# Optimization experiments

Hardware: AMD Instinct MI355X
Metric: run time of the kernel (lower is better)

The kernel has to match this reference:

```python
import jax, jax.numpy as jnp
import numpy as np


def topk_activation(x, k):
    # x: [B, L]; keep top-k per row, zeros elsewhere (torch.topk + scatter_)
    vals, idx = jax.lax.top_k(x, k)            # [B, k]
    rows = jnp.arange(x.shape[0])[:, None]     # [B, 1]
    return jnp.zeros_like(x).at[rows, idx].set(vals)


def setup_inputs() -> dict:
    key = jax.random.key(0)
    k0, k1, k2, k3 = jax.random.split(key, 4)
    B, n_in, n_lat = 4096, 768, 24576
    x = jax.random.normal(k0, (B, n_in), dtype=jnp.float32)
    b = jnp.zeros((n_in,), jnp.float32)
    W_enc = jax.random.normal(k1, (n_lat, n_in), dtype=jnp.float32) * 0.02
    b_enc = jnp.zeros((n_lat,), jnp.float32)
    W_dec = jax.random.normal(k2, (n_in, n_lat), dtype=jnp.float32) * 0.02
    # unit L2 norm per decoder column (as in _normalize_decoder)
    W_dec = W_dec / jnp.clip(jnp.linalg.norm(W_dec, axis=0, keepdims=True), 1e-8)
    miss_counts = jax.random.randint(k3, (n_lat,), 0, 2)  # ~half 'dead' (>=1)
    return {"x": x, "b": b, "W_enc": W_enc, "b_enc": b_enc, "W_dec": W_dec,
            "miss_counts": miss_counts, "k": 32, "aux_k": 512}


def reference(x, b, W_enc, b_enc, W_dec, miss_counts, k, aux_k):
    x_centered = x - b                                   # [B, n_in]
    alpha_pre = x_centered @ W_enc.T + b_enc             # [B, n_lat]
    alpha = topk_activation(alpha_pre, k)                # sparse code
    x_hat = alpha @ W_dec.T + b                          # dense decode
    fired_mask = alpha != 0
    # aux dead-feature path; dead_mask = miss_counts >= threshold(=1).
    # With the chosen miss_counts fill, dead count >> aux_k, so
    # min(aux_k, dead.sum()) == aux_k (static for jit).
    dead_mask = miss_counts >= 1                         # [n_lat]
    alpha_pre_dead = jnp.where(dead_mask[None, :], alpha_pre, -jnp.inf)
    alpha_aux = topk_activation(alpha_pre_dead, aux_k)
    aux_x_hat = alpha_aux @ W_dec.T + b
    return x_hat, alpha, fired_mask, aux_x_hat
```

## Files before the change

### kernel.cpp

```cpp
#include <hip/hip_runtime.h>
#include <math.h>

#define NB   4096
#define NIN  768
#define NLAT 24576
#define K2   768
#define KT2  12

#define BM 128
#define BN 128
#define BK 16
#define LDT 132

#define CAND_CAP 512
#define BAND_CAP 160
#define MAIN_CAP 64
#define AUX_CAP  1024
#define SELT     1024
#define GRP      6

#define CM_CAP 768
#define CA_CAP 1536
#define BB_CAP 256
#define BPSTRIDE (BAND_CAP + 4)

#define OFF_K16  0
#define OFF_REDF 49152
#define OFF_CTRL 49664
#define OFF_PCNT 49792
#define OFF_CKM  50176
#define OFF_CIM  52224
#define OFF_CKA  54272
#define OFF_CIA  56320
#define OFF_BIM  58368
#define OFF_BIA  59008
#define OFF_BVM  59648
#define OFF_BVA  60928
#define OFF_BSM  62208
#define OFF_BSA  62368
#define OFF_REDI 62528
#define SMEM_SEL 62592

typedef __bf16 bf16x8 __attribute__((ext_vector_type(8)));
typedef float  f32x4  __attribute__((ext_vector_type(4)));

__device__ __forceinline__ unsigned fkey(float f) {
  unsigned u = __float_as_uint(f);
  return u ^ ((unsigned)((int)u >> 31) | 0x80000000u);
}
__device__ __forceinline__ float keyinv(unsigned u) {
  unsigned s = (u & 0x80000000u) ? (u ^ 0x80000000u) : ~u;
  return __uint_as_float(s);
}
__device__ __forceinline__ float zup(float p) {
  p = fminf(fmaxf(p, 1e-7f), 0.5f);
  float t = sqrtf(-2.0f * logf(p));
  return t - (2.30753f + 0.27061f * t) / (1.0f + 0.99229f * t + 0.04481f * t * t);
}

#define GLOAD16(g, l) __builtin_amdgcn_global_load_lds( \
    (const __attribute__((address_space(1))) unsigned int*)(g), \
    (__attribute__((address_space(3))) unsigned int*)(l), 16, 0, 0)

__global__ __launch_bounds__(256) void k_deadbits(const int* __restrict__ miss,
                                                  unsigned* __restrict__ bits,
                                                  float* __restrict__ rowStats) {
  int j = blockIdx.x * 256 + threadIdx.x;
  unsigned long long b = __ballot(miss[j] >= 1);
  if ((threadIdx.x & 63) == 0) {
    int w = j >> 5;
    bits[w] = (unsigned)b;
    bits[w + 1] = (unsigned)(b >> 32);
  }
  if (j < 2 * NB) rowStats[j] = 0.0f;
}

__global__ __launch_bounds__(256) void k_ndead(const unsigned* __restrict__ bits,
                                               int* __restrict__ out) {
  __shared__ int w[4];
  int t = threadIdx.x;
  int c = 0;
  for (int i = t; i < NLAT / 32; i += 256) c += __popc(bits[i]);
#pragma unroll
  for (int o = 32; o; o >>= 1) c += __shfl_xor(c, o);
  if ((t & 63) == 0) w[t >> 6] = c;
  __syncthreads();
  if (t == 0) out[0] = w[0] + w[1] + w[2] + w[3];
}

__global__ __launch_bounds__(256) void k_rowstats(const float* __restrict__ apre,
                                                  float* __restrict__ rowStats) {
  const int r = blockIdx.x, t = threadIdx.x;
  const float4* rowp = (const float4*)(apre + (size_t)r * NLAT);
  float s1 = 0.f, s2 = 0.f;
  for (int g = t; g < NLAT / 4; g += 256) {
    float4 v = rowp[g];
    s1 += v.x + v.y + v.z + v.w;
    s2 += v.x * v.x + v.y * v.y + v.z * v.z + v.w * v.w;
  }
#pragma unroll
  for (int o = 32; o; o >>= 1) { s1 += __shfl_xor(s1, o); s2 += __shfl_xor(s2, o); }
  __shared__ float w1[4], w2[4];
  if ((t & 63) == 0) { w1[t >> 6] = s1; w2[t >> 6] = s2; }
  __syncthreads();
  if (t == 0) {
    rowStats[2 * r] = w1[0] + w1[1] + w1[2] + w1[3];
    rowStats[2 * r + 1] = w2[0] + w2[1] + w2[2] + w2[3];
  }
}

__global__ __launch_bounds__(256) void k_transpose(const float* __restrict__ src,
                                                   __bf16* __restrict__ dst) {
  __shared__ float tile[32][33];
  int bx = blockIdx.x * 32;
  int by = blockIdx.y * 32;
  int tx = threadIdx.x, ty = threadIdx.y;
  for (int i = ty; i < 32; i += 8)
    tile[i][tx] = src[(size_t)(by + i) * NLAT + bx + tx];
  __syncthreads();
  for (int i = ty; i < 32; i += 8)
    dst[(size_t)(bx + i) * NIN + by + tx] = (__bf16)tile[tx][i];
}

__global__ __launch_bounds__(256) void k_pack_a(const float* __restrict__ x,
    const float* __restrict__ bvec, __bf16* __restrict__ A2) {
  const int mt = blockIdx.x, kt = blockIdx.y, t = threadIdx.x;
  __bf16* out = A2 + (((size_t)mt * KT2 + kt) << 13);
#pragma unroll
  for (int i = 0; i < 32; ++i) {
    int idx = i * 256 + t;
    int r = idx >> 6, c2 = idx & 63;
    int kk = c2 ^ ((r & 7) << 3);
    int k = kt * 64 + kk;
    float v = x[(size_t)(mt * 128 + r) * NIN + k] - bvec[k];
    out[idx] = (__bf16)v;
  }
}

__global__ __launch_bounds__(256) void k_pack_b(const float* __restrict__ We,
    __bf16* __restrict__ B2) {
  const int nt = blockIdx.x, kt = blockIdx.y, t = threadIdx.x;
  __bf16* out = B2 + (((size_t)nt * KT2 + kt) << 13);
#pragma unroll
  for (int i = 0; i < 32; ++i) {
    int idx = i * 256 + t;
    int r = idx >> 6, c2 = idx & 63;
    int kk = c2 ^ ((r & 7) << 3);
    int k = kt * 64 + kk;
    float v = We[(size_t)(nt * 128 + r) * NIN + k];
    out[idx] = (__bf16)v;
  }
}

__global__ __launch_bounds__(256) void k_gemm_bf16(
    const __bf16* __restrict__ A2, const __bf16* __restrict__ B2,
    const float* __restrict__ be, float* __restrict__ apre,
    float* __restrict__ rowStats) {
  __shared__ char sA[16384];
  __shared__ char sB[16384];
  const int t = threadIdx.x;
  const int lane = t & 63, wave = t >> 6;
  int flat = blockIdx.y * 32 + blockIdx.x;
  int nf = (flat & 7) * 768 + (flat >> 3);
  const int mt = nf & 31, nt = nf >> 5;
  const int wm = wave >> 1, wn = wave & 1;

  int aoff[4][2], boff[4][2];
#pragma unroll
  for (int f = 0; f < 4; ++f) {
    int ra = wm * 64 + f * 16 + (lane & 15);
    int rb = wn * 64 + f * 16 + (lane & 15);
#pragma unroll
    for (int kk = 0; kk < 2; ++kk) {
      int c = kk * 64 + (lane >> 4) * 16;
      aoff[f][kk] = ra * 128 + (c ^ ((ra & 7) << 4));
      boff[f][kk] = rb * 128 + (c ^ ((rb & 7) << 4));
    }
  }
  f32x4 acc[4][4] = {};
  const char* gA = (const char*)(A2 + (((size_t)mt * KT2) << 13));
  const char* gB = (const char*)(B2 + (((size_t)nt * KT2) << 13));
  for (int kt = 0; kt < KT2; ++kt) {
    const char* tA = gA + ((size_t)kt << 14);
    const char* tB = gB + ((size_t)kt << 14);
#pragma unroll
    for (int i = 0; i < 4; ++i) {
      int chunk = (i * 4 + wave) * 1024;
      GLOAD16(tA + chunk + lane * 16, sA + chunk);
      GLOAD16(tB + chunk + lane * 16, sB + chunk);
    }
    __syncthreads();
#pragma unroll
    for (int kk = 0; kk < 2; ++kk) {
      bf16x8 a[4], b[4];
#pragma unroll
      for (int f = 0; f < 4; ++f) {
        a[f] = *(const bf16x8*)(sA + aoff[f][kk]);
        b[f] = *(const bf16x8*)(sB + boff[f][kk]);
      }
#pragma unroll
      for (int mi = 0; mi < 4; ++mi)
#pragma unroll
        for (int ni = 0; ni < 4; ++ni)
          acc[mi][ni] = __builtin_amdgcn_mfma_f32_16x16x32_bf16(a[mi], b[ni], acc[mi][ni], 0, 0, 0);
    }
    __syncthreads();
  }
  const int m0 = mt * 128 + wm * 64, n0 = nt * 128 + wn * 64;
  float ps1[16] = {}, ps2[16] = {};
#pragma unroll
  for (int ni = 0; ni < 4; ++ni) {
    int n = n0 + ni * 16 + (lane & 15);
    float bb = be[n];
#pragma unroll
    for (int mi = 0; mi < 4; ++mi) {
      int mbase = m0 + mi * 16 + (lane >> 4) * 4;
#pragma unroll
      for (int q = 0; q < 4; ++q) {
        float v = acc[mi][ni][q] + bb;
        apre[(size_t)(mbase + q) * NLAT + n] = v;
        ps1[mi * 4 + q] += v;
        ps2[mi * 4 + q] += v * v;
      }
    }
  }
#pragma unroll
  for (int i = 0; i < 16; ++i) {
#pragma unroll
    for (int o = 1; o < 16; o <<= 1) {
      ps1[i] += __shfl_xor(ps1[i], o);
      ps2[i] += __shfl_xor(ps2[i], o);
    }
  }
  if ((lane & 15) == 0) {
#pragma unroll
    for (int i = 0; i < 16; ++i) {
      int row = m0 + (i >> 2) * 16 + (lane >> 4) * 4 + (i & 3);
      atomicAdd(&rowStats[2 * row], ps1[i]);
      atomicAdd(&rowStats[2 * row + 1], ps2[i]);
    }
  }
}

__global__ __launch_bounds__(256) void k_encgemm_f32(
    const float* __restrict__ x, const float* __restrict__ bvec,
    const float* __restrict__ We, const float* __restrict__ be,
    float* __restrict__ apre) {
  __shared__ float As[BK][LDT];
  __shared__ float Bs[BK][LDT];
  const int t = threadIdx.x;
  const int m0 = blockIdx.x * BM;
  const int n0 = blockIdx.y * BN;
  const int lane = t & 63, wave = t >> 6;
  const int cn = ((wave & 1) * 8 + (lane & 7)) * 8;
  const int cm = ((wave >> 1) * 8 + (lane >> 3)) * 8;
  float acc[8][8] = {};
  const float* xb = x + (size_t)m0 * NIN;
  const float* wb = We + (size_t)n0 * NIN;
  for (int k0 = 0; k0 < NIN; k0 += BK) {
#pragma unroll
    for (int i = 0; i < 2; ++i) {
      int e = t + i * 256;
      int row = e >> 2, q = e & 3;
      float4 bv = *(const float4*)(bvec + k0 + q * 4);
      float4 av = *(const float4*)(xb + (size_t)row * NIN + k0 + q * 4);
      av.x -= bv.x; av.y -= bv.y; av.z -= bv.z; av.w -= bv.w;
      As[q * 4 + 0][row] = av.x; As[q * 4 + 1][row] = av.y;
      As[q * 4 + 2][row] = av.z; As[q * 4 + 3][row] = av.w;
      float4 wv = *(const float4*)(wb + (size_t)row * NIN + k0 + q * 4);
      Bs[q * 4 + 0][row] = wv.x; Bs[q * 4 + 1][row] = wv.y;
      Bs[q * 4 + 2][row] = wv.z; Bs[q * 4 + 3][row] = wv.w;
    }
    __syncthreads();
#pragma unroll
    for (int kk = 0; kk < BK; ++kk) {
      float a0[8], b0[8];
      *(float4*)&a0[0] = *(const float4*)&As[kk][cm];
      *(float4*)&a0[4] = *(const float4*)&As[kk][cm + 4];
      *(float4*)&b0[0] = *(const float4*)&Bs[kk][cn];
      *(float4*)&b0[4] = *(const float4*)&Bs[kk][cn + 4];
#pragma unroll
      for (int i = 0; i < 8; ++i)
#pragma unroll
        for (int j = 0; j < 8; ++j)
          acc[i][j] = fmaf(a0[i], b0[j], acc[i][j]);
    }
    __syncthreads();
  }
  float bb[8];
  *(float4*)&bb[0] = *(const float4*)(be + n0 + cn);
  *(float4*)&bb[4] = *(const float4*)(be + n0 + cn + 4);
#pragma unroll
  for (int i = 0; i < 8; ++i) {
    float4 v0 = make_float4(acc[i][0] + bb[0], acc[i][1] + bb[1],
                            acc[i][2] + bb[2], acc[i][3] + bb[3]);
    float4 v1 = make_float4(acc[i][4] + bb[4], acc[i][5] + bb[5],
                            acc[i][6] + bb[6], acc[i][7] + bb[7]);
    float* orow = apre + (size_t)(m0 + cm + i) * NLAT + n0 + cn;
    *(float4*)orow = v0;
    *(float4*)(orow + 4) = v1;
  }
}

__global__ __launch_bounds__(1024) void k_select17(
    const float* __restrict__ apre, const float* __restrict__ x,
    const float* __restrict__ bvec, const float* __restrict__ We,
    const float* __restrict__ be, const unsigned* __restrict__ dbits,
    const int* __restrict__ kptr, const int* __restrict__ akptr,
    const int* __restrict__ ndeadP, const float* __restrict__ rowStats,
    int* __restrict__ cnts, int* __restrict__ mIdxG, float* __restrict__ mValG,
    int* __restrict__ aIdxG, float* __restrict__ aValG,
    int* __restrict__ bandP, int* __restrict__ flags) {
  __shared__ int ctrl[24];
  __shared__ int histM[256];
  __shared__ int histA[256];
  __shared__ uint2 cM[CM_CAP];
  __shared__ uint2 cA[CA_CAP];
  __shared__ uint2 bbM[BB_CAP];
  __shared__ uint2 bbA[BB_CAP];
  __shared__ int biM[BAND_CAP];
  __shared__ int biA[BAND_CAP];
  __shared__ double bvM[BAND_CAP];
  __shared__ double bvA[BAND_CAP];
  __shared__ unsigned char bsM[BAND_CAP];
  __shared__ unsigned char bsA[BAND_CAP];
  unsigned* uctrl = (unsigned*)ctrl;

  const int t = threadIdx.x;
  const int r = blockIdx.x;
  const int lane = t & 63, wave = t >> 6;

  if (t < 24) ctrl[t] = 0;
  if (t >= 256 && t < 512) histM[t - 256] = 0;
  else if (t >= 512 && t < 768) histA[t - 512] = 0;
  __syncthreads();

  int kmain = kptr[0]; if (kmain > MAIN_CAP) kmain = MAIN_CAP;
  int kaux  = akptr[0]; if (kaux > AUX_CAP)  kaux  = AUX_CAP;
  const int ndead = ndeadP[0];
  int kauxE = kaux > ndead ? ndead : kaux;
  const bool mainOn = (kmain > 0);
  const bool auxOn  = (kauxE > 0);
  const float s1 = rowStats[2 * r], s2 = rowStats[2 * r + 1];
  const float mu = s1 / (float)NLAT;
  const float sg = sqrtf(fmaxf(s2 / (float)NLAT - mu * mu, 1e-20f));
  unsigned TkM = 0xFFFFFFFFu, TkA = 0xFFFFFFFFu;
  if (mainOn) TkM = fkey(mu + sg * zup(8.f * kmain / (float)NLAT));
  if (auxOn) {
    float facA = (3.f * kauxE > 1280.f) ? 2.f : 3.f;
    TkA = fkey(mu + sg * zup(facA * kauxE / (float)ndead));
  }

  const uint4* rowp = (const uint4*)(apre + (size_t)r * NLAT);
  unsigned mxM = 0u, mxA = 0u;
#pragma unroll
  for (int i = 0; i < GRP; ++i) {
    int g = t + SELT * i;
    uint4 rv = rowp[g];
    unsigned nb = (dbits[g >> 3] >> ((g & 7) * 4)) & 0xFu;
    float vs[4] = {__uint_as_float(rv.x), __uint_as_float(rv.y),
                   __uint_as_float(rv.z), __uint_as_float(rv.w)};
#pragma unroll
    for (int q = 0; q < 4; ++q) {
      unsigned kk = fkey(vs[q]);
      unsigned j = (unsigned)(4 * g + q);
      if (mainOn && kk >= TkM) {
        mxM = kk > mxM ? kk : mxM;
        int p = atomicAdd(&ctrl[0], 1);
        if (p < CM_CAP) { cM[p].x = kk; cM[p].y = j; }
      }
      if (auxOn && ((nb >> q) & 1u) && kk >= TkA) {
        mxA = kk > mxA ? kk : mxA;
        int p = atomicAdd(&ctrl[1], 1);
        if (p < CA_CAP) { cA[p].x = kk; cA[p].y = j; }
      }
    }
  }
#pragma unroll
  for (int o = 32; o; o >>= 1) {
    unsigned a = __shfl_xor(mxM, o); mxM = a > mxM ? a : mxM;
    unsigned b = __shfl_xor(mxA, o); mxA = b > mxA ? b : mxA;
  }
  if (lane == 0) { atomicMax(&uctrl[10], mxM); atomicMax(&uctrl[11], mxA); }
  __syncthreads();
  int ccM = ctrl[0], ccA = ctrl[1];
  bool ok = (!mainOn || (ccM >= kmain && ccM <= CM_CAP)) &&
            (!auxOn  || (ccA >= kauxE && ccA <= CA_CAP));
  if (!ok) { if (t == 0) flags[r] = 1; return; }
  if (!auxOn) ccA = 0;
  if (!mainOn) ccM = 0;
  unsigned MxM = uctrl[10], MxA = uctrl[11];
  float sclM = 255.0f / fmaxf((float)(MxM - TkM) + 1.0f, 1.0f);
  float sclA = 255.0f / fmaxf((float)(MxA - TkA) + 1.0f, 1.0f);

  for (int c = t; c < ccM; c += 1024) {
    int b = (int)((float)(cM[c].x - TkM) * sclM);
    b = b < 0 ? 0 : (b > 255 ? 255 : b);
    atomicAdd(&histM[b], 1);
  }
  for (int c = t; c < ccA; c += 1024) {
    int b = (int)((float)(cA[c].x - TkA) * sclA);
    b = b < 0 ? 0 : (b > 255 ? 255 : b);
    atomicAdd(&histA[b], 1);
  }
  __syncthreads();
  if (t == 0 && mainOn) {
    int above = 0, b = 0;
    for (int i = 255; i >= 0; --i) {
      if (above + histM[i] >= kmain) { b = i; break; }
      above += histM[i];
    }
    ctrl[12] = b; ctrl[13] = above;
  }
  if (t == 64 && auxOn) {
    int above = 0, b = 0;
    for (int i = 255; i >= 0; --i) {
      if (above + histA[i] >= kauxE) { b = i; break; }
      above += histA[i];
    }
    ctrl[14] = b; ctrl[15] = above;
  }
  __syncthreads();
  int bM = ctrl[12], aboveM = ctrl[13];
  int bA = ctrl[14], aboveA = ctrl[15];
  for (int c = t; c < ccM; c += 1024) {
    int b = (int)((float)(cM[c].x - TkM) * sclM);
    b = b < 0 ? 0 : (b > 255 ? 255 : b);
    if (b == bM) {
      int p = atomicAdd(&ctrl[16], 1);
      if (p < BB_CAP) bbM[p] = cM[c];
    }
  }
  for (int c = t; c < ccA; c += 1024) {
    int b = (int)((float)(cA[c].x - TkA) * sclA);
    b = b < 0 ? 0 : (b > 255 ? 255 : b);
    if (b == bA) {
      int p = atomicAdd(&ctrl[17], 1);
      if (p < BB_CAP) bbA[p] = cA[c];
    }
  }
  __syncthreads();
  int nbM = ctrl[16], nbA = ctrl[17];
  if ((mainOn && nbM > BB_CAP) || (auxOn && nbA > BB_CAP)) {
    if (t == 0) flags[r] = 1;
    return;
  }
  if (!mainOn) nbM = 0;
  if (!auxOn) nbA = 0;
  if (t < nbM) {
    uint2 e = bbM[t];
    int rank = 0;
    for (int qq = 0; qq < nbM; ++qq) {
      uint2 f = bbM[qq];
      rank += (f.x > e.x || (f.x == e.x && (int)f.y < (int)e.y)) ? 1 : 0;
    }
    if (rank == kmain - aboveM - 1) ctrl[2] = (int)e.x;
  }
  if (t >= 512 && t - 512 < nbA) {
    uint2 e = bbA[t - 512];
    int rank = 0;
    for (int qq = 0; qq < nbA; ++qq) {
      uint2 f = bbA[qq];
      rank += (f.x > e.x || (f.x == e.x && (int)f.y < (int)e.y)) ? 1 : 0;
    }
    if (rank == kauxE - aboveA - 1) ctrl[3] = (int)e.x;
  }
  __syncthreads();

  float VsM = keyinv((unsigned)ctrl[2]);
  float epsM = 1.5e-2f + 2e-3f * fabsf(VsM);
  unsigned KhiBM = mainOn ? fkey(VsM + epsM) : 0xFFFFFFFFu;
  unsigned KloBM = mainOn ? fkey(VsM - epsM) : 0xFFFFFFFFu;
  float VsA = keyinv((unsigned)ctrl[3]);
  float epsA = 1.5e-2f + 2e-3f * fabsf(VsA);
  unsigned KhiBA = auxOn ? fkey(VsA + epsA) : 0xFFFFFFFFu;
  unsigned KloBA = auxOn ? fkey(VsA - epsA) : 0xFFFFFFFFu;
  for (int c = t; c < ccM; c += 1024) {
    unsigned kk = cM[c].x;
    if (kk > KhiBM) atomicAdd(&ctrl[4], 1);
    else if (kk >= KloBM) {
      int p = atomicAdd(&ctrl[5], 1);
      if (p < BAND_CAP) biM[p] = (int)cM[c].y;
    }
  }
  for (int c = t; c < ccA; c += 1024) {
    unsigned kk = cA[c].x;
    if (kk > KhiBA) atomicAdd(&ctrl[6], 1);
    else if (kk >= KloBA) {
      int p = atomicAdd(&ctrl[7], 1);
      if (p < BAND_CAP) biA[p] = (int)cA[c].y;
    }
  }
  __syncthreads();
  if ((mainOn && ctrl[5] > BAND_CAP) || (auxOn && ctrl[7] > BAND_CAP)) {
    if (t == 0) flags[r] = 1;
    return;
  }
  if (t == 0) flags[r] = 0;
  int nAbM = ctrl[4], bcM = ctrl[5];
  int nAbA = ctrl[6], bcA = ctrl[7];
  if (!mainOn) bcM = 0;
  if (!auxOn) bcA = 0;
  int needBM = kmain - nAbM; if (needBM < 0) needBM = 0; if (needBM > bcM) needBM = bcM;
  int needBA = kauxE - nAbA; if (needBA < 0) needBA = 0; if (needBA > bcA) needBA = bcA;

  {
    const float* xr = x + (size_t)r * NIN;
    float xb[NIN / 64];
#pragma unroll
    for (int jj = 0; jj < NIN / 64; ++jj) {
      int col = lane + 64 * jj;
      xb[jj] = xr[col] - bvec[col];
    }
    int tot = bcM + bcA;
    for (int m = wave; m < tot; m += 16) {
      int j = (m < bcM) ? biM[m] : biA[m - bcM];
      const float* wr = We + (size_t)j * NIN;
      double s = 0.0;
#pragma unroll
      for (int jj = 0; jj < NIN / 64; ++jj)
        s += (double)xb[jj] * (double)wr[lane + 64 * jj];
#pragma unroll
      for (int o = 32; o; o >>= 1) s += __shfl_xor(s, o);
      if (lane == 0) {
        if (m < bcM) bvM[m] = s + (double)be[j];
        else bvA[m - bcM] = s + (double)be[j];
      }
    }
  }
  __syncthreads();
  if (t < bcM) {
    double vi = bvM[t]; int ii = biM[t];
    double tie = fabs(vi) * 4e-8 + 1e-12;
    int rank = 0;
    for (int qq = 0; qq < bcM; ++qq) {
      double d = bvM[qq] - vi;
      rank += ((fabs(d) <= tie) ? (biM[qq] < ii) : (d > 0.0)) ? 1 : 0;
    }
    bsM[t] = (rank < needBM) ? 1 : 0;
  }
  if (t >= 512 && t - 512 < bcA) {
    int tt = t - 512;
    double vi = bvA[tt]; int ii = biA[tt];
    double tie = fabs(vi) * 4e-8 + 1e-12;
    int rank = 0;
    for (int qq = 0; qq < bcA; ++qq) {
      double d = bvA[qq] - vi;
      rank += ((fabs(d) <= tie) ? (biA[qq] < ii) : (d > 0.0)) ? 1 : 0;
    }
    bsA[tt] = (rank < needBA) ? 1 : 0;
  }
  __syncthreads();

  for (int c = t; c < ccM; c += 1024) {
    unsigned kk = cM[c].x; int j = (int)cM[c].y;
    bool sel = kk > KhiBM;
    if (!sel && kk >= KloBM) {
      for (int m2 = 0; m2 < bcM; ++m2)
        if (biM[m2] == j) { sel = bsM[m2] != 0; break; }
    }
    float v = keyinv(kk);
    if (sel && v != 0.0f) {
      int p = atomicAdd(&ctrl[8], 1);
      if (p < MAIN_CAP) { mIdxG[r * MAIN_CAP + p] = j; mValG[r * MAIN_CAP + p] = v; }
    }
  }
  for (int c = t; c < ccA; c += 1024) {
    unsigned kk = cA[c].x; int j = (int)cA[c].y;
    bool sel = kk > KhiBA;
    if (!sel && kk >= KloBA) {
      for (int m2 = 0; m2 < bcA; ++m2)
        if (biA[m2] == j) { sel = bsA[m2] != 0; break; }
    }
    float v = keyinv(kk);
    if (sel && v != 0.0f) {
      int p = atomicAdd(&ctrl[9], 1);
      if (p < AUX_CAP) { aIdxG[r * AUX_CAP + p] = j; aValG[r * AUX_CAP + p] = v; }
    }
  }
  __syncthreads();
  int* bp = bandP + (size_t)r * BPSTRIDE;
  if (t == 0) {
    cnts[2 * r] = ctrl[8] < MAIN_CAP ? ctrl[8] : MAIN_CAP;
    cnts[2 * r + 1] = auxOn ? (ctrl[9] < AUX_CAP ? ctrl[9] : AUX_CAP) : 0;
    bp[0] = (int)KhiBM; bp[1] = (int)KloBM; bp[2] = bcM;
  }
  if (t < bcM) bp[3 + t] = (biM[t] << 1) | (int)bsM[t];
}

__global__ __launch_bounds__(256) void k_emit(
    const float* apre, const int* __restrict__ flags,
    const int* __restrict__ bandP, float* __restrict__ alpha, float* mask) {
  const int bid = blockIdx.x;
  const int r = bid / 3, c = bid % 3;
  if (flags[r]) return;
  __shared__ int hdr[3];
  __shared__ int bent[BAND_CAP];
  const int t = threadIdx.x;
  const int* bp = bandP + (size_t)r * BPSTRIDE;
  if (t < 3) hdr[t] = bp[t];
  __syncthreads();
  int bc = hdr[2];
  if (t < bc) bent[t] = bp[3 + t];
  __syncthreads();
  unsigned KhiB = (unsigned)hdr[0], KloB = (unsigned)hdr[1];
  const float4* src = (const float4*)(apre + (size_t)r * NLAT) + c * 2048;
  float4* adst = (float4*)(alpha + (size_t)r * NLAT) + c * 2048;
  float4* mdst = (float4*)(mask + (size_t)r * NLAT) + c * 2048;
  const int ebase = c * 8192;
#pragma unroll
  for (int i = 0; i < 8; ++i) {
    int g = t + 256 * i;
    float4 v4 = src[g];
    float vs[4] = {v4.x, v4.y, v4.z, v4.w};
    float av[4], mv[4];
#pragma unroll
    for (int q = 0; q < 4; ++q) {
      float v = vs[q];
      unsigned kk = fkey(v);
      int j = ebase + 4 * g + q;
      bool sel = kk > KhiB;
      if (!sel && kk >= KloB) {
        for (int m = 0; m < bc; ++m)
          if ((bent[m] >> 1) == j) { sel = (bent[m] & 1) != 0; break; }
      }
      av[q] = sel ? v : 0.0f;
      mv[q] = (sel && v != 0.0f) ? 1.0f : 0.0f;
    }
    adst[g] = make_float4(av[0], av[1], av[2], av[3]);
    mdst[g] = make_float4(mv[0], mv[1], mv[2], mv[3]);
  }
}

__global__ __launch_bounds__(SELT) void k_selectFB(
    const float* apre, const float* __restrict__ x,
    const float* __restrict__ bvec, const float* __restrict__ We,
    const float* __restrict__ be, const unsigned* __restrict__ dbits,
    const int* __restrict__ kptr, const int* __restrict__ akptr,
    float* __restrict__ alpha, float* mask,
    int* __restrict__ cnts, int* __restrict__ mIdxG, float* __restrict__ mValG,
    int* __restrict__ aIdxG, float* __restrict__ aValG,
    const int* __restrict__ flags) {
  if (flags[blockIdx.x] == 0) return;
  extern __shared__ char smem[];
  uint2*    keys2 = (uint2*)(smem + OFF_K16);
  float*    redF  = (float*)(smem + OFF_REDF);
  int*      redI  = (int*)(smem + OFF_REDI);
  int*      ctrl  = (int*)(smem + OFF_CTRL);
  float*    ctrlF = (float*)(smem + OFF_CTRL);
  int*      pcnt  = (int*)(smem + OFF_PCNT);
  unsigned* ckM   = (unsigned*)(smem + OFF_CKM);
  int*      ciM   = (int*)(smem + OFF_CIM);
  unsigned* ckA   = (unsigned*)(smem + OFF_CKA);
  int*      ciA   = (int*)(smem + OFF_CIA);
  int*      biM   = (int*)(smem + OFF_BIM);
  int*      biA   = (int*)(smem + OFF_BIA);
  double*   bvM   = (double*)(smem + OFF_BVM);
  double*   bvA   = (double*)(smem + OFF_BVA);
  unsigned char* bsM = (unsigned char*)(smem + OFF_BSM);
  unsigned char* bsA = (unsigned char*)(smem + OFF_BSA);

  const int t = threadIdx.x;
  const int r = blockIdx.x;
  const int lane = t & 63, wave = t >> 6;

  if (t < 96) pcnt[t] = 0;
  else if (t < 108) ctrl[t - 96] = 0;

  const uint4* rowp = (const uint4*)(apre + (size_t)r * NLAT);
  const float* rowf = apre + (size_t)r * NLAT;
  unsigned dm = 0;
  float s1 = 0.f, s2 = 0.f;
  float vmxA = -INFINITY, vmnA = INFINITY, vmxD = -INFINITY, vmnD = INFINITY;
#pragma unroll
  for (int i = 0; i < GRP; ++i) {
    int g = t + SELT * i;
    uint4 rv = rowp[g];
    unsigned nb = (dbits[g >> 3] >> ((g & 7) * 4)) & 0xFu;
    dm |= nb << (4 * i);
    float vs[4] = {__uint_as_float(rv.x), __uint_as_float(rv.y),
                   __uint_as_float(rv.z), __uint_as_float(rv.w)};
    unsigned k16[4];
#pragma unroll
    for (int q = 0; q < 4; ++q) {
      float v = vs[q];
      k16[q] = fkey(v) >> 16;
      s1 += v; s2 += v * v;
      vmxA = fmaxf(vmxA, v); vmnA = fminf(vmnA, v);
      if ((nb >> q) & 1u) { vmxD = fmaxf(vmxD, v); vmnD = fminf(vmnD, v); }
    }
    uint2 kp2;
    kp2.x = k16[0] | (k16[1] << 16);
    kp2.y = k16[2] | (k16[3] << 16);
    keys2[g] = kp2;
  }
  int nd = __popc(dm & 0xFFFFFFu);
#pragma unroll
  for (int o = 32; o; o >>= 1) {
    s1 += __shfl_xor(s1, o); s2 += __shfl_xor(s2, o);
    vmxA = fmaxf(vmxA, __shfl_xor(vmxA, o)); vmnA = fminf(vmnA, __shfl_xor(vmnA, o));
    vmxD = fmaxf(vmxD, __shfl_xor(vmxD, o)); vmnD = fminf(vmnD, __shfl_xor(vmnD, o));
    nd += __shfl_xor(nd, o);
  }
  if (lane == 0) {
    float* rf = redF + wave * 8;
    rf[0] = s1; rf[1] = s2; rf[2] = vmxA; rf[3] = vmnA; rf[4] = vmxD; rf[5] = vmnD;
    redI[wave] = nd;
  }
  __syncthreads();
  if (wave == 0) {
    float a0 = 0.f, a1 = 0.f, a2 = -INFINITY, a3 = INFINITY, a4 = -INFINITY, a5 = INFINITY;
    int a6 = 0;
    if (lane < 16) {
      const float* rf = redF + lane * 8;
      a0 = rf[0]; a1 = rf[1]; a2 = rf[2]; a3 = rf[3]; a4 = rf[4]; a5 = rf[5];
      a6 = redI[lane];
    }
#pragma unroll
    for (int o = 32; o; o >>= 1) {
      a0 += __shfl_xor(a0, o); a1 += __shfl_xor(a1, o);
      a2 = fmaxf(a2, __shfl_xor(a2, o)); a3 = fminf(a3, __shfl_xor(a3, o));
// ... 275 lines not shown
          for (int m2 = 0; m2 < bcM; ++m2)
            if (biM[m2] == j) { selM = bsM[m2] != 0; break; }
        }
        bool nz = selM && (v != 0.0f);
        av[q] = selM ? v : 0.0f;
        mv[q] = nz ? 1.0f : 0.0f;
        if (nz) {
          int p = atomicAdd(&ctrl[8], 1);
          if (p < MAIN_CAP) { mIdxG[r * MAIN_CAP + p] = j; mValG[r * MAIN_CAP + p] = v; }
        }
        if (auxOn && ((nb >> q) & 1u)) {
          bool selA = kk > KhiBA;
          if (!selA && kk >= KloBA) {
            for (int m2 = 0; m2 < bcA; ++m2)
              if (biA[m2] == j) { selA = bsA[m2] != 0; break; }
          }
          if (selA && v != 0.0f) {
            int p = atomicAdd(&ctrl[9], 1);
            if (p < AUX_CAP) { aIdxG[r * AUX_CAP + p] = j; aValG[r * AUX_CAP + p] = v; }
          }
        }
      }
      arow[g] = make_float4(av[0], av[1], av[2], av[3]);
      mrow[g] = make_float4(mv[0], mv[1], mv[2], mv[3]);
    }
  }
  __syncthreads();
  if (t == 0) {
    cnts[2 * r] = ctrl[8] < MAIN_CAP ? ctrl[8] : MAIN_CAP;
    cnts[2 * r + 1] = auxOn ? (ctrl[9] < AUX_CAP ? ctrl[9] : AUX_CAP) : 0;
  }
}

__global__ __launch_bounds__(256) void k_decode(
    const int* __restrict__ cnts, const int* __restrict__ mIdxG,
    const float* __restrict__ mValG, const int* __restrict__ aIdxG,
    const float* __restrict__ aValG, const float* __restrict__ bvec,
    const __bf16* __restrict__ Wt, const float* __restrict__ Wd,
    float* __restrict__ xhat, float* __restrict__ auxo) {
  const int r = blockIdx.x, t = threadIdx.x;
  __shared__ int sMi[MAIN_CAP];
  __shared__ float sMv[MAIN_CAP];
  __shared__ int sAi[AUX_CAP];
  __shared__ float sAv[AUX_CAP];
  int kc = cnts[2 * r], ac = cnts[2 * r + 1];
  if (t < MAIN_CAP && t < kc) { sMi[t] = mIdxG[r * MAIN_CAP + t]; sMv[t] = mValG[r * MAIN_CAP + t]; }
  for (int i = t; i < ac; i += 256) { sAi[i] = aIdxG[r * AUX_CAP + i]; sAv[i] = aValG[r * AUX_CAP + i]; }
  __syncthreads();

  float o0 = 0.f, o1 = 0.f, o2 = 0.f;
  float a0 = 0.f, a1 = 0.f, a2 = 0.f;
  if (Wt) {
    int i = 0;
    for (; i + 4 <= kc; i += 4) {
      int i0 = sMi[i], i1 = sMi[i + 1], i2 = sMi[i + 2], i3 = sMi[i + 3];
      float v0 = sMv[i], v1 = sMv[i + 1], v2 = sMv[i + 2], v3 = sMv[i + 3];
      const __bf16* p0 = Wt + (size_t)i0 * NIN;
      const __bf16* p1 = Wt + (size_t)i1 * NIN;
      const __bf16* p2 = Wt + (size_t)i2 * NIN;
      const __bf16* p3 = Wt + (size_t)i3 * NIN;
      float w00 = p0[t], w01 = p0[t + 256], w02 = p0[t + 512];
      float w10 = p1[t], w11 = p1[t + 256], w12 = p1[t + 512];
      float w20 = p2[t], w21 = p2[t + 256], w22 = p2[t + 512];
      float w30 = p3[t], w31 = p3[t + 256], w32 = p3[t + 512];
      o0 = fmaf(v0, w00, o0); o1 = fmaf(v0, w01, o1); o2 = fmaf(v0, w02, o2);
      o0 = fmaf(v1, w10, o0); o1 = fmaf(v1, w11, o1); o2 = fmaf(v1, w12, o2);
      o0 = fmaf(v2, w20, o0); o1 = fmaf(v2, w21, o1); o2 = fmaf(v2, w22, o2);
      o0 = fmaf(v3, w30, o0); o1 = fmaf(v3, w31, o1); o2 = fmaf(v3, w32, o2);
    }
    for (; i < kc; ++i) {
      const __bf16* p = Wt + (size_t)sMi[i] * NIN;
      float v = sMv[i];
      o0 = fmaf(v, (float)p[t], o0);
      o1 = fmaf(v, (float)p[t + 256], o1);
      o2 = fmaf(v, (float)p[t + 512], o2);
    }
    i = 0;
    for (; i + 4 <= ac; i += 4) {
      int i0 = sAi[i], i1 = sAi[i + 1], i2 = sAi[i + 2], i3 = sAi[i + 3];
      float v0 = sAv[i], v1 = sAv[i + 1], v2 = sAv[i + 2], v3 = sAv[i + 3];
      const __bf16* p0 = Wt + (size_t)i0 * NIN;
      const __bf16* p1 = Wt + (size_t)i1 * NIN;
      const __bf16* p2 = Wt + (size_t)i2 * NIN;
      const __bf16* p3 = Wt + (size_t)i3 * NIN;
      float w00 = p0[t], w01 = p0[t + 256], w02 = p0[t + 512];
      float w10 = p1[t], w11 = p1[t + 256], w12 = p1[t + 512];
      float w20 = p2[t], w21 = p2[t + 256], w22 = p2[t + 512];
      float w30 = p3[t], w31 = p3[t + 256], w32 = p3[t + 512];
      a0 = fmaf(v0, w00, a0); a1 = fmaf(v0, w01, a1); a2 = fmaf(v0, w02, a2);
      a0 = fmaf(v1, w10, a0); a1 = fmaf(v1, w11, a1); a2 = fmaf(v1, w12, a2);
      a0 = fmaf(v2, w20, a0); a1 = fmaf(v2, w21, a1); a2 = fmaf(v2, w22, a2);
      a0 = fmaf(v3, w30, a0); a1 = fmaf(v3, w31, a1); a2 = fmaf(v3, w32, a2);
    }
    for (; i < ac; ++i) {
      const __bf16* p = Wt + (size_t)sAi[i] * NIN;
      float v = sAv[i];
      a0 = fmaf(v, (float)p[t], a0);
      a1 = fmaf(v, (float)p[t + 256], a1);
      a2 = fmaf(v, (float)p[t + 512], a2);
    }
  } else {
    for (int i = 0; i < kc; ++i) {
      float v = sMv[i]; int ix = sMi[i];
      o0 = fmaf(v, Wd[(size_t)t * NLAT + ix], o0);
      o1 = fmaf(v, Wd[(size_t)(t + 256) * NLAT + ix], o1);
      o2 = fmaf(v, Wd[(size_t)(t + 512) * NLAT + ix], o2);
    }
    for (int i = 0; i < ac; ++i) {
      float v = sAv[i]; int ix = sAi[i];
      a0 = fmaf(v, Wd[(size_t)t * NLAT + ix], a0);
      a1 = fmaf(v, Wd[(size_t)(t + 256) * NLAT + ix], a1);
      a2 = fmaf(v, Wd[(size_t)(t + 512) * NLAT + ix], a2);
    }
  }
  float b0 = bvec[t], b1 = bvec[t + 256], b2 = bvec[t + 512];
  xhat[(size_t)r * NIN + t] = o0 + b0;
  xhat[(size_t)r * NIN + t + 256] = o1 + b1;
  xhat[(size_t)r * NIN + t + 512] = o2 + b2;
  auxo[(size_t)r * NIN + t] = a0 + b0;
  auxo[(size_t)r * NIN + t + 256] = a1 + b1;
  auxo[(size_t)r * NIN + t + 512] = a2 + b2;
}

extern "C" void kernel_launch(void* const* d_in, const int* in_sizes, int n_in,
                              void* d_out, int out_size, void* d_ws, size_t ws_size,
                              hipStream_t stream) {
  const float* x  = (const float*)d_in[0];
  const float* bv = (const float*)d_in[1];
  const float* We = (const float*)d_in[2];
  const float* be = (const float*)d_in[3];
  const float* Wd = (const float*)d_in[4];
  const int* miss = (const int*)d_in[5];
  const int* kp   = (const int*)d_in[6];
  const int* akp  = (const int*)d_in[7];

  float* out   = (float*)d_out;
  float* xhat  = out;
  float* alpha = out + (size_t)3145728;
  float* apre  = out + (size_t)103809024;
  float* auxo  = out + (size_t)204472320;

  char* wsb = (char*)d_ws;
  size_t o = 0;
  unsigned* dbits = (unsigned*)(wsb + o); o += 65536;
  int*   cnts  = (int*)(wsb + o); o += 65536;
  int*   mIdxG = (int*)(wsb + o); o += (size_t)NB * MAIN_CAP * 4;
  float* mValG = (float*)(wsb + o); o += (size_t)NB * MAIN_CAP * 4;
  int*   aIdxG = (int*)(wsb + o); o += (size_t)NB * AUX_CAP * 4;
  float* aValG = (float*)(wsb + o); o += (size_t)NB * AUX_CAP * 4;
  int*   bandP = (int*)(wsb + o); o += (size_t)NB * BPSTRIDE * 4;
  int*   flags = (int*)(wsb + o); o += 65536;
  int*   ndead = (int*)(wsb + o); o += 65536;
  float* rowStats = (float*)(wsb + o); o += (size_t)NB * 2 * 4;
  size_t offWt = o;
  size_t offA2 = offWt + (size_t)NLAT * NIN * 2;
  size_t offB2 = offA2 + (size_t)NB * K2 * 2;
  size_t needFull = offB2 + (size_t)NLAT * K2 * 2;
  bool haveWt   = ws_size >= offA2;
  bool haveFull = ws_size >= needFull;
  __bf16* Wt = haveWt ? (__bf16*)(wsb + offWt) : nullptr;
  __bf16* A2 = (__bf16*)(wsb + offA2);
  __bf16* B2 = (__bf16*)(wsb + offB2);

  k_deadbits<<<96, 256, 0, stream>>>(miss, dbits, rowStats);
  k_ndead<<<1, 256, 0, stream>>>(dbits, ndead);
  if (haveFull) {
    k_pack_a<<<dim3(32, KT2), 256, 0, stream>>>(x, bv, A2);
    k_pack_b<<<dim3(192, KT2), 256, 0, stream>>>(We, B2);
  }
  if (haveWt)
    k_transpose<<<dim3(NLAT / 32, NIN / 32), dim3(32, 8), 0, stream>>>(Wd, Wt);

  if (haveFull) {
    k_gemm_bf16<<<dim3(32, 192), 256, 0, stream>>>(A2, B2, be, apre, rowStats);
  } else {
    k_encgemm_f32<<<dim3(NB / BM, NLAT / BN), 256, 0, stream>>>(x, bv, We, be, apre);
    k_rowstats<<<NB, 256, 0, stream>>>(apre, rowStats);
  }

  k_select17<<<NB, 1024, 0, stream>>>(apre, x, bv, We, be, dbits, kp, akp, ndead,
                                      rowStats, cnts, mIdxG, mValG, aIdxG, aValG,
                                      bandP, flags);
  k_selectFB<<<NB, SELT, SMEM_SEL, stream>>>(apre, x, bv, We, be, dbits, kp, akp,
                                             alpha, apre, cnts, mIdxG, mValG,
                                             aIdxG, aValG, flags);
  k_emit<<<NB * 3, 256, 0, stream>>>(apre, flags, bandP, alpha, apre);
  k_decode<<<NB, 256, 0, stream>>>(cnts, mIdxG, mValG, aIdxG, aValG, bv,
                                   Wt, Wd, xhat, auxo);
}
```

Baseline: 1.463 ms.

## Split row selection into multi-block candidate extraction and per-row ranking kernels

Replaces the single 1024-thread per-row select kernel with two kernels. The first scans each row with three 256-thread blocks and appends threshold-passing candidates to global buffers, using global atomics for per-row counts and maxima. The second kernel runs 512 threads per row, copies those candidates into shared memory and does the histogram, band and ranking logic as before. The aim is better occupancy and parallelism for the memory-bound row scan. In exchange it adds global atomic contention on per-row counters, extra global traffic for the candidate buffers, one more launch, and half as many waves for the band dot products.

```diff
diff --git a/kernel.cpp b/kernel.cpp
--- a/kernel.cpp
+++ b/kernel.cpp
@@ -64,7 +64,8 @@
 
 __global__ __launch_bounds__(256) void k_deadbits(const int* __restrict__ miss,
                                                   unsigned* __restrict__ bits,
-                                                  float* __restrict__ rowStats) {
+                                                  float* __restrict__ rowStats,
+                                                  int* __restrict__ gmeta) {
   int j = blockIdx.x * 256 + threadIdx.x;
   unsigned long long b = __ballot(miss[j] >= 1);
   if ((threadIdx.x & 63) == 0) {
@@ -73,6 +74,7 @@
     bits[w + 1] = (unsigned)(b >> 32);
   }
   if (j < 2 * NB) rowStats[j] = 0.0f;
+  if (j < 4 * NB) gmeta[j] = 0;
 }
 
 __global__ __launch_bounds__(256) void k_ndead(const unsigned* __restrict__ bits,
@@ -302,38 +304,14 @@
   }
 }
 
-__global__ __launch_bounds__(1024) void k_select17(
-    const float* __restrict__ apre, const float* __restrict__ x,
-    const float* __restrict__ bvec, const float* __restrict__ We,
-    const float* __restrict__ be, const unsigned* __restrict__ dbits,
+__global__ __launch_bounds__(256) void k_extract(
+    const float* __restrict__ apre, const unsigned* __restrict__ dbits,
     const int* __restrict__ kptr, const int* __restrict__ akptr,
     const int* __restrict__ ndeadP, const float* __restrict__ rowStats,
-    int* __restrict__ cnts, int* __restrict__ mIdxG, float* __restrict__ mValG,
-    int* __restrict__ aIdxG, float* __restrict__ aValG,
-    int* __restrict__ bandP, int* __restrict__ flags) {
-  __shared__ int ctrl[24];
-  __shared__ int histM[256];
-  __shared__ int histA[256];
-  __shared__ uint2 cM[CM_CAP];
-  __shared__ uint2 cA[CA_CAP];
-  __shared__ uint2 bbM[BB_CAP];
-  __shared__ uint2 bbA[BB_CAP];
-  __shared__ int biM[BAND_CAP];
-  __shared__ int biA[BAND_CAP];
-  __shared__ double bvM[BAND_CAP];
-  __shared__ double bvA[BAND_CAP];
-  __shared__ unsigned char bsM[BAND_CAP];
-  __shared__ unsigned char bsA[BAND_CAP];
-  unsigned* uctrl = (unsigned*)ctrl;
-
+    int* __restrict__ gmeta, uint2* __restrict__ gcM, uint2* __restrict__ gcA) {
+  const int bid = blockIdx.x;
+  const int r = bid / 3, c = bid % 3;
   const int t = threadIdx.x;
-  const int r = blockIdx.x;
-  const int lane = t & 63, wave = t >> 6;
-
-  if (t < 24) ctrl[t] = 0;
-  if (t >= 256 && t < 512) histM[t - 256] = 0;
-  else if (t >= 512 && t < 768) histA[t - 512] = 0;
-  __syncthreads();
 
   int kmain = kptr[0]; if (kmain > MAIN_CAP) kmain = MAIN_CAP;
   int kaux  = akptr[0]; if (kaux > AUX_CAP)  kaux  = AUX_CAP;
@@ -351,55 +329,126 @@
     TkA = fkey(mu + sg * zup(facA * kauxE / (float)ndead));
   }
 
-  const uint4* rowp = (const uint4*)(apre + (size_t)r * NLAT);
-  unsigned mxM = 0u, mxA = 0u;
-#pragma unroll
-  for (int i = 0; i < GRP; ++i) {
-    int g = t + SELT * i;
-    uint4 rv = rowp[g];
-    unsigned nb = (dbits[g >> 3] >> ((g & 7) * 4)) & 0xFu;
+  int* cntM = gmeta;
+  int* cntA = gmeta + NB;
+  unsigned* mxM = (unsigned*)(gmeta + 2 * NB);
+  unsigned* mxA = (unsigned*)(gmeta + 3 * NB);
+  uint2* lcM = gcM + (size_t)r * CM_CAP;
+  uint2* lcA = gcA + (size_t)r * CA_CAP;
+
+  const uint4* src = (const uint4*)(apre + (size_t)r * NLAT) + c * 2048;
+  const int ebase = c * 8192;
+  unsigned wmxM = 0u, wmxA = 0u;
+#pragma unroll
+  for (int i = 0; i < 8; ++i) {
+    int g = t + 256 * i;
+    uint4 rv = src[g];
+    int j0 = ebase + 4 * g;
+    unsigned nb = (dbits[j0 >> 5] >> (j0 & 31)) & 0xFu;
     float vs[4] = {__uint_as_float(rv.x), __uint_as_float(rv.y),
                    __uint_as_float(rv.z), __uint_as_float(rv.w)};
 #pragma unroll
     for (int q = 0; q < 4; ++q) {
       unsigned kk = fkey(vs[q]);
-      unsigned j = (unsigned)(4 * g + q);
+      unsigned j = (unsigned)(j0 + q);
       if (mainOn && kk >= TkM) {
-        mxM = kk > mxM ? kk : mxM;
-        int p = atomicAdd(&ctrl[0], 1);
-        if (p < CM_CAP) { cM[p].x = kk; cM[p].y = j; }
+        wmxM = kk > wmxM ? kk : wmxM;
+        int p = atomicAdd(&cntM[r], 1);
+        if (p < CM_CAP) { lcM[p].x = kk; lcM[p].y = j; }
       }
       if (auxOn && ((nb >> q) & 1u) && kk >= TkA) {
-        mxA = kk > mxA ? kk : mxA;
-        int p = atomicAdd(&ctrl[1], 1);
-        if (p < CA_CAP) { cA[p].x = kk; cA[p].y = j; }
+        wmxA = kk > wmxA ? kk : wmxA;
+        int p = atomicAdd(&cntA[r], 1);
+        if (p < CA_CAP) { lcA[p].x = kk; lcA[p].y = j; }
       }
     }
   }
 #pragma unroll
   for (int o = 32; o; o >>= 1) {
-    unsigned a = __shfl_xor(mxM, o); mxM = a > mxM ? a : mxM;
-    unsigned b = __shfl_xor(mxA, o); mxA = b > mxA ? b : mxA;
-  }
-  if (lane == 0) { atomicMax(&uctrl[10], mxM); atomicMax(&uctrl[11], mxA); }
-  __syncthreads();
-  int ccM = ctrl[0], ccA = ctrl[1];
+    unsigned a = __shfl_xor(wmxM, o); wmxM = a > wmxM ? a : wmxM;
+    unsigned b = __shfl_xor(wmxA, o); wmxA = b > wmxA ? b : wmxA;
+  }
+  if ((t & 63) == 0) {
+    if (wmxM) atomicMax(&mxM[r], wmxM);
+    if (wmxA) atomicMax(&mxA[r], wmxA);
+  }
+}
+
+__global__ __launch_bounds__(512) void k_rank(
+    const float* __restrict__ x, const float* __restrict__ bvec,
+    const float* __restrict__ We, const float* __restrict__ be,
+    const int* __restrict__ kptr, const int* __restrict__ akptr,
+    const int* __restrict__ ndeadP, const float* __restrict__ rowStats,
+    const int* __restrict__ gmeta, const uint2* __restrict__ gcM,
+    const uint2* __restrict__ gcA,
+    int* __restrict__ cnts, int* __restrict__ mIdxG, float* __restrict__ mValG,
+    int* __restrict__ aIdxG, float* __restrict__ aValG,
+    int* __restrict__ bandP, int* __restrict__ flags) {
+  __shared__ int ctrl[24];
+  __shared__ int histM[256];
+  __shared__ int histA[256];
+  __shared__ uint2 lcM[CM_CAP];
+  __shared__ uint2 lcA[CA_CAP];
+  __shared__ uint2 bbM[BB_CAP];
+  __shared__ uint2 bbA[BB_CAP];
+  __shared__ int biM[BAND_CAP];
+  __shared__ int biA[BAND_CAP];
+  __shared__ double bvM[BAND_CAP];
+  __shared__ double bvA[BAND_CAP];
+  __shared__ unsigned char bsM[BAND_CAP];
+  __shared__ unsigned char bsA[BAND_CAP];
+
+  const int t = threadIdx.x;
+  const int r = blockIdx.x;
+  const int lane = t & 63, wave = t >> 6;
+
+  if (t < 24) ctrl[t] = 0;
+  if (t >= 24 && t < 280) histM[t - 24] = 0;
+  else if (t >= 280 && t < 512 ) histA[t - 280] = 0;
+  __syncthreads();
+  if (t < 24) {}
+  if (t < 24 + 24) {}
+  if (t < 24) {}
+  if (t < 24) histA[232 + t] = 0;
+  __syncthreads();
+
+  int kmain = kptr[0]; if (kmain > MAIN_CAP) kmain = MAIN_CAP;
+  int kaux  = akptr[0]; if (kaux > AUX_CAP)  kaux  = AUX_CAP;
+  const int ndead = ndeadP[0];
+  int kauxE = kaux > ndead ? ndead : kaux;
+  const bool mainOn = (kmain > 0);
+  const bool auxOn  = (kauxE > 0);
+  const float s1 = rowStats[2 * r], s2 = rowStats[2 * r + 1];
+  const float mu = s1 / (float)NLAT;
+  const float sg = sqrtf(fmaxf(s2 / (float)NLAT - mu * mu, 1e-20f));
+  unsigned TkM = 0xFFFFFFFFu, TkA = 0xFFFFFFFFu;
+  if (mainOn) TkM = fkey(mu + sg * zup(8.f * kmain / (float)NLAT));
+  if (auxOn) {
+    float facA = (3.f * kauxE > 1280.f) ? 2.f : 3.f;
+    TkA = fkey(mu + sg * zup(facA * kauxE / (float)ndead));
+  }
+
+  int ccM = gmeta[r], ccA = gmeta[NB + r];
+  unsigned MxM = ((const unsigned*)(gmeta + 2 * NB))[r];
+  unsigned MxA = ((const unsigned*)(gmeta + 3 * NB))[r];
   bool ok = (!mainOn || (ccM >= kmain && ccM <= CM_CAP)) &&
             (!auxOn  || (ccA >= kauxE && ccA <= CA_CAP));
   if (!ok) { if (t == 0) flags[r] = 1; return; }
   if (!auxOn) ccA = 0;
   if (!mainOn) ccM = 0;
-  unsigned MxM = uctrl[10], MxA = uctrl[11];
+  for (int i = t; i < ccM; i += 512) lcM[i] = gcM[(size_t)r * CM_CAP + i];
+  for (int i = t; i < ccA; i += 512) lcA[i] = gcA[(size_t)r * CA_CAP + i];
+  __syncthreads();
   float sclM = 255.0f / fmaxf((float)(MxM - TkM) + 1.0f, 1.0f);
   float sclA = 255.0f / fmaxf((float)(MxA - TkA) + 1.0f, 1.0f);
 
-  for (int c = t; c < ccM; c += 1024) {
-    int b = (int)((float)(cM[c].x - TkM) * sclM);
+  for (int c = t; c < ccM; c += 512) {
+    int b = (int)((float)(lcM[c].x - TkM) * sclM);
     b = b < 0 ? 0 : (b > 255 ? 255 : b);
     atomicAdd(&histM[b], 1);
   }
-  for (int c = t; c < ccA; c += 1024) {
-    int b = (int)((float)(cA[c].x - TkA) * sclA);
+  for (int c = t; c < ccA; c += 512) {
+    int b = (int)((float)(lcA[c].x - TkA) * sclA);
     b = b < 0 ? 0 : (b > 255 ? 255 : b);
     atomicAdd(&histA[b], 1);
   }
@@ -423,20 +472,20 @@
   __syncthreads();
   int bM = ctrl[12], aboveM = ctrl[13];
   int bA = ctrl[14], aboveA = ctrl[15];
-  for (int c = t; c < ccM; c += 1024) {
-    int b = (int)((float)(cM[c].x - TkM) * sclM);
+  for (int c = t; c < ccM; c += 512) {
+    int b = (int)((float)(lcM[c].x - TkM) * sclM);
     b = b < 0 ? 0 : (b > 255 ? 255 : b);
     if (b == bM) {
       int p = atomicAdd(&ctrl[16], 1);
-      if (p < BB_CAP) bbM[p] = cM[c];
-    }
-  }
-  for (int c = t; c < ccA; c += 1024) {
-    int b = (int)((float)(cA[c].x - TkA) * sclA);
+      if (p < BB_CAP) bbM[p] = lcM[c];
+    }
+  }
+  for (int c = t; c < ccA; c += 512) {
+    int b = (int)((float)(lcA[c].x - TkA) * sclA);
     b = b < 0 ? 0 : (b > 255 ? 255 : b);
     if (b == bA) {
       int p = atomicAdd(&ctrl[17], 1);
-      if (p < BB_CAP) bbA[p] = cA[c];
+      if (p < BB_CAP) bbA[p] = lcA[c];
     }
   }
   __syncthreads();
@@ -456,8 +505,8 @@
     }
     if (rank == kmain - aboveM - 1) ctrl[2] = (int)e.x;
   }
-  if (t >= 512 && t - 512 < nbA) {
-    uint2 e = bbA[t - 512];
+  if (t >= 256 && t - 256 < nbA) {
+    uint2 e = bbA[t - 256];
     int rank = 0;
     for (int qq = 0; qq < nbA; ++qq) {
       uint2 f = bbA[qq];
@@ -475,20 +524,20 @@
   float epsA = 1.5e-2f + 2e-3f * fabsf(VsA);
   unsigned KhiBA = auxOn ? fkey(VsA + epsA) : 0xFFFFFFFFu;
   unsigned KloBA = auxOn ? fkey(VsA - epsA) : 0xFFFFFFFFu;
-  for (int c = t; c < ccM; c += 1024) {
-    unsigned kk = cM[c].x;
+  for (int c = t; c < ccM; c += 512) {
+    unsigned kk = lcM[c].x;
     if (kk > KhiBM) atomicAdd(&ctrl[4], 1);
     else if (kk >= KloBM) {
       int p = atomicAdd(&ctrl[5], 1);
-      if (p < BAND_CAP) biM[p] = (int)cM[c].y;
-    }
-  }
-  for (int c = t; c < ccA; c += 1024) {
-    unsigned kk = cA[c].x;
+      if (p < BAND_CAP) biM[p] = (int)lcM[c].y;
+    }
+  }
+  for (int c = t; c < ccA; c += 512) {
+    unsigned kk = lcA[c].x;
     if (kk > KhiBA) atomicAdd(&ctrl[6], 1);
     else if (kk >= KloBA) {
       int p = atomicAdd(&ctrl[7], 1);
-      if (p < BAND_CAP) biA[p] = (int)cA[c].y;
+      if (p < BAND_CAP) biA[p] = (int)lcA[c].y;
     }
   }
   __syncthreads();
@@ -513,7 +562,7 @@
       xb[jj] = xr[col] - bvec[col];
     }
     int tot = bcM + bcA;
-    for (int m = wave; m < tot; m += 16) {
+    for (int m = wave; m < tot; m += 8) {
       int j = (m < bcM) ? biM[m] : biA[m - bcM];
       const float* wr = We + (size_t)j * NIN;
       double s = 0.0;
@@ -539,8 +588,8 @@
     }
     bsM[t] = (rank < needBM) ? 1 : 0;
   }
-  if (t >= 512 && t - 512 < bcA) {
-    int tt = t - 512;
+  if (t >= 256 && t - 256 < bcA) {
+    int tt = t - 256;
     double vi = bvA[tt]; int ii = biA[tt];
     double tie = fabs(vi) * 4e-8 + 1e-12;
     int rank = 0;
@@ -552,8 +601,8 @@
   }
   __syncthreads();
 
-  for (int c = t; c < ccM; c += 1024) {
-    unsigned kk = cM[c].x; int j = (int)cM[c].y;
+  for (int c = t; c < ccM; c += 512) {
+    unsigned kk = lcM[c].x; int j = (int)lcM[c].y;
     bool sel = kk > KhiBM;
     if (!sel && kk >= KloBM) {
       for (int m2 = 0; m2 < bcM; ++m2)
@@ -565,8 +614,8 @@
       if (p < MAIN_CAP) { mIdxG[r * MAIN_CAP + p] = j; mValG[r * MAIN_CAP + p] = v; }
     }
   }
-  for (int c = t; c < ccA; c += 1024) {
-    unsigned kk = cA[c].x; int j = (int)cA[c].y;
+  for (int c = t; c < ccA; c += 512) {
+    unsigned kk = lcA[c].x; int j = (int)lcA[c].y;
     bool sel = kk > KhiBA;
     if (!sel && kk >= KloBA) {
       for (int m2 = 0; m2 < bcA; ++m2)
@@ -1148,6 +1197,9 @@
   int*   flags = (int*)(wsb + o); o += 65536;
   int*   ndead = (int*)(wsb + o); o += 65536;
   float* rowStats = (float*)(wsb + o); o += (size_t)NB * 2 * 4;
+  int*   gmeta = (int*)(wsb + o); o += (size_t)NB * 4 * 4;
+  uint2* gcM = (uint2*)(wsb + o); o += (size_t)NB * CM_CAP * 8;
+  uint2* gcA = (uint2*)(wsb + o); o += (size_t)NB * CA_CAP * 8;
   size_t offWt = o;
   size_t offA2 = offWt + (size_t)NLAT * NIN * 2;
   size_t offB2 = offA2 + (size_t)NB * K2 * 2;
@@ -1158,7 +1210,7 @@
   __bf16* A2 = (__bf16*)(wsb + offA2);
   __bf16* B2 = (__bf16*)(wsb + offB2);
 
-  k_deadbits<<<96, 256, 0, stream>>>(miss, dbits, rowStats);
+  k_deadbits<<<96, 256, 0, stream>>>(miss, dbits, rowStats, gmeta);
   k_ndead<<<1, 256, 0, stream>>>(dbits, ndead);
   if (haveFull) {
     k_pack_a<<<dim3(32, KT2), 256, 0, stream>>>(x, bv, A2);
@@ -1174,9 +1226,11 @@
     k_rowstats<<<NB, 256, 0, stream>>>(apre, rowStats);
   }
 
-  k_select17<<<NB, 1024, 0, stream>>>(apre, x, bv, We, be, dbits, kp, akp, ndead,
-                                      rowStats, cnts, mIdxG, mValG, aIdxG, aValG,
-                                      bandP, flags);
+  k_extract<<<NB * 3, 256, 0, stream>>>(apre, dbits, kp, akp, ndead, rowStats,
+                                        gmeta, gcM, gcA);
+  k_rank<<<NB, 512, 0, stream>>>(x, bv, We, be, kp, akp, ndead, rowStats,
+                                 gmeta, gcM, gcA, cnts, mIdxG, mValG,
+                                 aIdxG, aValG, bandP, flags);
   k_selectFB<<<NB, SELT, SMEM_SEL, stream>>>(apre, x, bv, We, be, dbits, kp, akp,
                                              alpha, apre, cnts, mIdxG, mValG,
                                              aIdxG, aValG, flags);
```

After: 1.834 ms. +25.4%, slower.
